# Kernel tuning notes

Hardware: AMD Instinct MI355X
Metric: run time of the kernel (lower is better)

Reference implementation:

```python
import jax, jax.numpy as jnp
import numpy as np


def setup_inputs() -> dict:
    key = jax.random.key(0)
    k1, k2 = jax.random.split(key)
    emb_in = jax.random.normal(k1, (2048, 32), dtype=jnp.float32)
    sum_weights = jax.random.normal(k2, (2048,), dtype=jnp.float32)
    return {"emb_in": emb_in, "sum_weights": sum_weights}


def reference(emb_in, sum_weights):
    # emb_in: [n, f], sum_weights: [n]
    n, f = emb_in.shape
    # a[k] = emb_in[k // n]  (each row repeated n times consecutively)
    a = jnp.repeat(emb_in, n, axis=0)          # [n*n, f]
    # b[k] = emb_in[k % n]   (whole tensor tiled n times)
    b = jnp.tile(emb_in, (n, 1))               # [n*n, f]
    # weights column matches b: w[k] = sum_weights[k % n]
    w = jnp.tile(sum_weights[:, None], (n, 1)) # [n*n, 1]
    sample = jnp.concatenate((a, b, w), axis=1)  # [n*n, 2*f + 1]
    return sample
```

## Files before the change

kernel.cpp:

```cpp
#include <hip/hip_runtime.h>


#define NROWS 2048u
#define WAVE_ROWS 16u
#define WAVE_FLOATS (WAVE_ROWS * 65u)
#define WAVE_F4 (WAVE_FLOATS / 4u)
#define TILE_ROWS 64u
#define TILE_F4 (TILE_ROWS * 65u / 4u)

typedef float f32x4 __attribute__((ext_vector_type(4)));

__global__ __launch_bounds__(256) void expand_wave(
    const float* __restrict__ emb,
    const float* __restrict__ sw,
    f32x4* __restrict__ out)
{
    __shared__ __align__(16) float lds[4 * WAVE_FLOATS];

    const unsigned tid  = threadIdx.x;
    const unsigned wave = tid >> 6;
    const unsigned lane = tid & 63u;

    const unsigned r0 = blockIdx.x * TILE_ROWS + wave * WAVE_ROWS;
    const unsigned i  = r0 >> 11;
    const unsigned j0 = r0 & (NROWS - 1u);

    float* wlds = lds + wave * WAVE_FLOATS;

    const f32x4* embj = (const f32x4*)(emb + (size_t)j0 * 32u);
    const f32x4 b0 = embj[lane];
    const f32x4 b1 = embj[lane + 64u];

    {
        unsigned g = lane;
        unsigned d = (g >> 3) * 65u + 32u + (g & 7u) * 4u;
        wlds[d + 0u] = b0.x; wlds[d + 1u] = b0.y;
        wlds[d + 2u] = b0.z; wlds[d + 3u] = b0.w;
        g = lane + 64u;
        d = (g >> 3) * 65u + 32u + (g & 7u) * 4u;
        wlds[d + 0u] = b1.x; wlds[d + 1u] = b1.y;
        wlds[d + 2u] = b1.z; wlds[d + 3u] = b1.w;
    }

    const float vi = emb[i * 32u + (lane & 31u)];
    const unsigned rbase = (lane >> 5) * 8u;
#pragma unroll
    for (unsigned rp = 0; rp < 8u; ++rp)
        wlds[(rbase + rp) * 65u + (lane & 31u)] = vi;

    if (lane < WAVE_ROWS)
        wlds[lane * 65u + 64u] = sw[j0 + lane];

    asm volatile("s_waitcnt lgkmcnt(0)" ::: "memory");

    const f32x4* wlds4 = (const f32x4*)wlds;
    const unsigned obase = blockIdx.x * TILE_F4 + wave * WAVE_F4;
#pragma unroll
    for (unsigned p = 0; p < 4u; ++p) {
        const unsigned idx = p * 64u + lane;
        __builtin_nontemporal_store(wlds4[idx], &out[obase + idx]);
    }
    if (lane < 4u) {
        const unsigned idx = 256u + lane;
        __builtin_nontemporal_store(wlds4[idx], &out[obase + idx]);
    }
}

extern "C" void kernel_launch(void* const* d_in, const int* in_sizes, int n_in,
                              void* d_out, int out_size, void* d_ws, size_t ws_size,
                              hipStream_t stream) {
    const float* emb = (const float*)d_in[0];
    const float* sw  = (const float*)d_in[1];
    f32x4* out       = (f32x4*)d_out;

    const unsigned tiles = (NROWS * NROWS) / TILE_ROWS;
    expand_wave<<<dim3(tiles), dim3(256), 0, stream>>>(emb, sw, out);
}
```

Measured before the change: 213.0 us.

## Make each wave loop over eight slabs with double-buffered LDS prefetch

Each wave now handles 128 output rows as eight 16-row slabs instead of a single slab, which cuts the grid by eight. The a-row broadcast is written once into both LDS buffers. The b-rows and weights for the next slab are loaded while the current slab is stored, which amortises launch and setup cost and overlaps global loads with nontemporal stores. In exchange it doubles per-wave LDS use, reduces the number of blocks available for latency hiding, and relies on implicit wave-level LDS ordering with no explicit waitcnt.

```diff
diff --git a/kernel.cpp b/kernel.cpp
--- a/kernel.cpp
+++ b/kernel.cpp
@@ -2,67 +2,85 @@
 
 
 #define NROWS 2048u
-#define WAVE_ROWS 16u
-#define WAVE_FLOATS (WAVE_ROWS * 65u)
-#define WAVE_F4 (WAVE_FLOATS / 4u)
-#define TILE_ROWS 64u
-#define TILE_F4 (TILE_ROWS * 65u / 4u)
+#define BLOCK_ROWS 512u
+#define WAVE_ROWS 128u
+#define SLAB_ROWS 16u
+#define NSLABS 8u
+#define SLAB_FLOATS (SLAB_ROWS * 65u)
+#define SLAB_F4 (SLAB_FLOATS / 4u)
 
 typedef float f32x4 __attribute__((ext_vector_type(4)));
 
-__global__ __launch_bounds__(256) void expand_wave(
+__global__ __launch_bounds__(256) void expand_pipe(
     const float* __restrict__ emb,
     const float* __restrict__ sw,
     f32x4* __restrict__ out)
 {
-    __shared__ __align__(16) float lds[4 * WAVE_FLOATS];
+    __shared__ __align__(16) float lds[4][2][SLAB_FLOATS];
 
     const unsigned tid  = threadIdx.x;
     const unsigned wave = tid >> 6;
     const unsigned lane = tid & 63u;
 
-    const unsigned r0 = blockIdx.x * TILE_ROWS + wave * WAVE_ROWS;
+    const unsigned r0 = blockIdx.x * BLOCK_ROWS + wave * WAVE_ROWS;
     const unsigned i  = r0 >> 11;
     const unsigned j0 = r0 & (NROWS - 1u);
-
-    float* wlds = lds + wave * WAVE_FLOATS;
-
-    const f32x4* embj = (const f32x4*)(emb + (size_t)j0 * 32u);
-    const f32x4 b0 = embj[lane];
-    const f32x4 b1 = embj[lane + 64u];
-
-    {
-        unsigned g = lane;
-        unsigned d = (g >> 3) * 65u + 32u + (g & 7u) * 4u;
-        wlds[d + 0u] = b0.x; wlds[d + 1u] = b0.y;
-        wlds[d + 2u] = b0.z; wlds[d + 3u] = b0.w;
-        g = lane + 64u;
-        d = (g >> 3) * 65u + 32u + (g & 7u) * 4u;
-        wlds[d + 0u] = b1.x; wlds[d + 1u] = b1.y;
-        wlds[d + 2u] = b1.z; wlds[d + 3u] = b1.w;
-    }
 
     const float vi = emb[i * 32u + (lane & 31u)];
     const unsigned rbase = (lane >> 5) * 8u;
 #pragma unroll
-    for (unsigned rp = 0; rp < 8u; ++rp)
-        wlds[(rbase + rp) * 65u + (lane & 31u)] = vi;
+    for (unsigned b = 0; b < 2u; ++b)
+#pragma unroll
+        for (unsigned rp = 0; rp < 8u; ++rp)
+            lds[wave][b][(rbase + rp) * 65u + (lane & 31u)] = vi;
 
-    if (lane < WAVE_ROWS)
-        wlds[lane * 65u + 64u] = sw[j0 + lane];
+    const unsigned d0 = (lane >> 3) * 65u + 32u + (lane & 7u) * 4u;
 
-    asm volatile("s_waitcnt lgkmcnt(0)" ::: "memory");
+    {
+        const f32x4* ej = (const f32x4*)(emb + (size_t)j0 * 32u);
+        const f32x4 pa = ej[lane];
+        const f32x4 pb = ej[lane + 64u];
+        const float ps = sw[j0 + (lane & 15u)];
+        float* B = &lds[wave][0][0];
+        B[d0 + 0u] = pa.x; B[d0 + 1u] = pa.y;
+        B[d0 + 2u] = pa.z; B[d0 + 3u] = pa.w;
+        B[d0 + 520u + 0u] = pb.x; B[d0 + 520u + 1u] = pb.y;
+        B[d0 + 520u + 2u] = pb.z; B[d0 + 520u + 3u] = pb.w;
+        if (lane < 16u) B[lane * 65u + 64u] = ps;
+    }
 
-    const f32x4* wlds4 = (const f32x4*)wlds;
-    const unsigned obase = blockIdx.x * TILE_F4 + wave * WAVE_F4;
 #pragma unroll
-    for (unsigned p = 0; p < 4u; ++p) {
-        const unsigned idx = p * 64u + lane;
-        __builtin_nontemporal_store(wlds4[idx], &out[obase + idx]);
-    }
-    if (lane < 4u) {
-        const unsigned idx = 256u + lane;
-        __builtin_nontemporal_store(wlds4[idx], &out[obase + idx]);
+    for (unsigned s = 0; s < NSLABS; ++s) {
+        const unsigned cur = s & 1u;
+
+        f32x4 pa, pb;
+        float ps = 0.0f;
+        if (s + 1u < NSLABS) {
+            const f32x4* ej =
+                (const f32x4*)(emb + (size_t)(j0 + (s + 1u) * SLAB_ROWS) * 32u);
+            pa = ej[lane];
+            pb = ej[lane + 64u];
+            ps = sw[j0 + (s + 1u) * SLAB_ROWS + (lane & 15u)];
+        }
+
+        const f32x4* L4 = (const f32x4*)&lds[wave][cur][0];
+        const unsigned obase = ((r0 + s * SLAB_ROWS) >> 4) * SLAB_F4;
+#pragma unroll
+        for (unsigned p = 0; p < 4u; ++p)
+            __builtin_nontemporal_store(L4[p * 64u + lane],
+                                        &out[obase + p * 64u + lane]);
+        if (lane < 4u)
+            __builtin_nontemporal_store(L4[256u + lane],
+                                        &out[obase + 256u + lane]);
+
+        if (s + 1u < NSLABS) {
+            float* B = &lds[wave][cur ^ 1u][0];
+            B[d0 + 0u] = pa.x; B[d0 + 1u] = pa.y;
+            B[d0 + 2u] = pa.z; B[d0 + 3u] = pa.w;
+            B[d0 + 520u + 0u] = pb.x; B[d0 + 520u + 1u] = pb.y;
+            B[d0 + 520u + 2u] = pb.z; B[d0 + 520u + 3u] = pb.w;
+            if (lane < 16u) B[lane * 65u + 64u] = ps;
+        }
     }
 }
 
@@ -73,6 +91,6 @@
     const float* sw  = (const float*)d_in[1];
     f32x4* out       = (f32x4*)d_out;
 
-    const unsigned tiles = (NROWS * NROWS) / TILE_ROWS;
-    expand_wave<<<dim3(tiles), dim3(256), 0, stream>>>(emb, sw, out);
+    const unsigned blocks = (NROWS * NROWS) / BLOCK_ROWS;
+    expand_pipe<<<dim3(blocks), dim3(256), 0, stream>>>(emb, sw, out);
 }
```

Measured after the change: 207.1 us. 1.03x faster.
